# Performance work log

Measured on AMD Instinct MI355X. Metric: run time of the kernel, lower is better.

Reference implementation:

```python
import jax, jax.numpy as jnp
import numpy as np

# Default DigitCaps config: reduced_votes=False, iter=1, softmax=False, tanh_like=False,
# l_thetas=[1.0], lr_som=1.0, radical=False, no normalization, no winner-ratio bookkeeping.
H, Wd, INPUT_F, INPUT_D = 12, 12, 32, 8
C, D, M = 10, 8, 4          # num_out_caps, vector_depth, transf_mat_for_each_caps
LR, THETA = 1.0, 1.0


def setup_inputs() -> dict:
    key = jax.random.key(0)
    k1, k2, k3 = jax.random.split(key, 3)
    B = 128
    inputs = jax.random.normal(k1, (B, H, Wd, INPUT_F, INPUT_D), dtype=jnp.float32)
    J = H * Wd * INPUT_F  # 4608 positions
    # he_normal over fan_in = INPUT_D
    W = jax.random.normal(k2, (J, INPUT_D, D * M), dtype=jnp.float32) * jnp.sqrt(2.0 / INPUT_D)
    digit_caps = jax.random.uniform(k3, (C, D), minval=-1.0, maxval=1.0, dtype=jnp.float32)
    return {"inputs": inputs, "W": W, "digit_caps": digit_caps}


def reference(inputs, W, digit_caps):
    B = inputs.shape[0]
    J = H * Wd * INPUT_F
    x = inputs.reshape(B, J, INPUT_D)
    # per-position transform: [B,J,input_d] x [J,input_d,D*M] -> [B,J,D*M]
    u = jnp.einsum('bji,jik->bjk', x, W)
    N = J * M
    u = u.reshape(B, N, D)  # votes (broadcast over C instead of tiling)

    # similarities[b,n,c] = <u[b,n], digit_caps[c]>
    sims = jnp.einsum('bnd,cd->bnc', u, digit_caps)
    winners = jnp.argmax(sims, axis=-1)  # [B, N] int

    # sparse_updates = one_hot(winners) * (u - digit_caps) * lr * theta;
    # updates = mean over (B, N). Computed via segment-sum (honors winner sparsity).
    flat_w = winners.reshape(-1)
    flat_u = u.reshape(-1, D)
    seg_u = jax.ops.segment_sum(flat_u, flat_w, num_segments=C)          # [C, D]
    counts = jnp.zeros((C,), jnp.float32).at[flat_w].add(1.0)            # [C]
    denom = jnp.float32(B * N)
    updates = (seg_u - counts[:, None] * digit_caps) * (LR * THETA) / denom

    digit_caps_new = digit_caps + updates  # assign_add happens before final sims

    sims_final = jnp.einsum('bnd,cd->bnc', u, digit_caps_new)
    output = jnp.mean(sims_final, axis=-2)  # [B, C]
    return output, digit_caps_new
```

## Files before the change

### kernel.cpp

```cpp
#include <hip/hip_runtime.h>


#define J_POS 4608
#define SEGSTRIDE 97
#define NSEG 32
#define SSTRIDE 513
#define NSREP 8
#define NVOTES 18432.0f
#define DENOM  2359296.0f
#define SEG_SCALE 32768.0f
#define INV_SEG_SCALE 3.0517578125e-5f
#define OFF_PART_SEG 64
#define OFF_PART_S   110656
#define OFF_S_FINAL  700480
#define OFF_SEG_PART_LL 350752

__global__ __launch_bounds__(256) void votes_kernel(
    const float* __restrict__ x,
    const float* __restrict__ w,
    const float* __restrict__ dc,
    int* __restrict__ part_seg,
    int* __restrict__ part_s,
    int* __restrict__ done)
{
    __shared__ int seg_lds[NSEG * SEGSTRIDE];
    __shared__ int s_lds[NSREP * SSTRIDE];

    const int t  = threadIdx.x;
    const int jg = blockIdx.x >> 1;
    const int h  = blockIdx.x & 1;
    const int j0 = jg * 8;

    if (blockIdx.x == 0 && t == 0) *done = 0;

    for (int i = t; i < NSEG * SEGSTRIDE; i += 256) seg_lds[i] = 0;
    for (int i = t; i < NSREP * SSTRIDE; i += 256) s_lds[i] = 0;

    const int jj   = t >> 5;
    const int m    = (t >> 3) & 3;
    const int brow = t & 7;
    const int j = j0 + jj;

    float4 wra[8], wrb[8];
    {
        const float* wp = w + (size_t)j * 256 + m * 8;
        #pragma unroll
        for (int i = 0; i < 8; ++i) {
            wra[i] = *(const float4*)(wp + i * 32);
            wrb[i] = *(const float4*)(wp + i * 32 + 4);
        }
    }
    float4 dca[10], dcb[10];
    #pragma unroll
    for (int c = 0; c < 10; ++c) {
        dca[c] = *(const float4*)(dc + c * 8);
        dcb[c] = *(const float4*)(dc + c * 8 + 4);
    }

    int* const segp = &seg_lds[((t >> 1) & (NSEG - 1)) * SEGSTRIDE];
    int* const sp = &s_lds[((t >> 3) & (NSREP - 1)) * SSTRIDE];

    __syncthreads();

    const int bbase = h * 64 + brow;
    float4 nx0, nx1, mx0, mx1;
    {
        const float* xp = x + ((size_t)bbase * J_POS + j) * 8;
        nx0 = *(const float4*)xp; nx1 = *(const float4*)(xp + 4);
        const float* xq = x + ((size_t)(bbase + 8) * J_POS + j) * 8;
        mx0 = *(const float4*)xq; mx1 = *(const float4*)(xq + 4);
    }

    #pragma unroll 1
    for (int it = 0; it < 8; ++it) {
        const int bl = it * 8 + brow;
        const float4 x0 = nx0, x1 = nx1;
        nx0 = mx0; nx1 = mx1;
        if (it < 6) {
            const float* xp = x + ((size_t)(bbase + (it + 2) * 8) * J_POS + j) * 8;
            mx0 = *(const float4*)xp;
            mx1 = *(const float4*)(xp + 4);
        }
        const float xf[8] = {x0.x,x0.y,x0.z,x0.w,x1.x,x1.y,x1.z,x1.w};

        float u[8] = {0,0,0,0,0,0,0,0};
        #pragma unroll
        for (int i = 0; i < 8; ++i) {
            const float xi = xf[i];
            u[0] += xi * wra[i].x; u[1] += xi * wra[i].y;
            u[2] += xi * wra[i].z; u[3] += xi * wra[i].w;
            u[4] += xi * wrb[i].x; u[5] += xi * wrb[i].y;
            u[6] += xi * wrb[i].z; u[7] += xi * wrb[i].w;
        }

        float best = -3.402823466e38f;
        int bc = 0;
        #pragma unroll
        for (int c = 0; c < 10; ++c) {
            const float sim = u[0]*dca[c].x + u[1]*dca[c].y + u[2]*dca[c].z + u[3]*dca[c].w
                            + u[4]*dcb[c].x + u[5]*dcb[c].y + u[6]*dcb[c].z + u[7]*dcb[c].w;
            if (sim > best) { best = sim; bc = c; }
        }

        const int o = bc * 9;
        const int sb = bl * 8;
        #pragma unroll
        for (int d = 0; d < 8; ++d) {
            const int q = __float2int_rn(u[d] * SEG_SCALE);
            atomicAdd(&segp[o + d], q);
            atomicAdd(&sp[sb + d], q);
        }
        atomicAdd(&segp[o + 8], 1);
    }

    __syncthreads();

    if (t < 90) {
        int v = 0;
        #pragma unroll
        for (int r = 0; r < NSEG; ++r) v += seg_lds[r * SEGSTRIDE + t];
        part_seg[blockIdx.x * 96 + t] = v;
    }
    #pragma unroll
    for (int e = t; e < 512; e += 256) {
        int v = 0;
        #pragma unroll
        for (int r = 0; r < NSREP; ++r) v += s_lds[r * SSTRIDE + e];
        part_s[(size_t)blockIdx.x * 512 + e] = v;
    }
}

__global__ __launch_bounds__(256) void reduce_final_kernel(
    const int* __restrict__ part_seg,
    const int* __restrict__ part_s,
    float* __restrict__ s_final,
    long long* __restrict__ seg_part,
    int* __restrict__ done,
    const float* __restrict__ dc,
    float* __restrict__ out)
{
    __shared__ long long red[64][5];
    __shared__ long long segred[2][96];
    __shared__ float dcn[80];
    __shared__ float sf[1024];
    __shared__ int lastflag;

    const int t = threadIdx.x;
    const int bid = blockIdx.x;

    if (bid < 16) {
        const int g0 = bid * 64;
        const int h = g0 >> 9;
        const int gl = t & 63, chunk = t >> 6;
        const int col = (g0 + gl) & 511;
        long long acc = 0;
        #pragma unroll 8
        for (int i = chunk * 144; i < chunk * 144 + 144; ++i)
            acc += part_s[(size_t)(2 * i + h) * 512 + col];
        red[gl][chunk] = acc;
        __syncthreads();
        if (t < 64) {
            const long long v = red[t][0] + red[t][1] + red[t][2] + red[t][3];
            __hip_atomic_store(&s_final[g0 + t], (float)v * INV_SEG_SCALE,
                               __ATOMIC_RELAXED, __HIP_MEMORY_SCOPE_AGENT);
        }
    } else {
        const int p = bid - 16;
        if (t < 192) {
            const int o = t % 96, rc = t / 96;
            long long acc = 0;
            const int r0 = p * 288 + rc * 144;
            #pragma unroll 8
            for (int i = r0; i < r0 + 144; ++i)
                acc += part_seg[(size_t)i * 96 + o];
            segred[rc][o] = acc;
        }
        __syncthreads();
        if (t < 96)
            __hip_atomic_store(&seg_part[p * 96 + t], segred[0][t] + segred[1][t],
                               __ATOMIC_RELAXED, __HIP_MEMORY_SCOPE_AGENT);
    }

    __threadfence();
    __syncthreads();
    if (t == 0) lastflag = (atomicAdd(done, 1) == 19) ? 1 : 0;
    __syncthreads();
    if (!lastflag) return;
    __threadfence();

    #pragma unroll
    for (int r = 0; r < 4; ++r) {
        const int i = r * 256 + t;
        const float v = __hip_atomic_load(&s_final[i], __ATOMIC_RELAXED,
                                          __HIP_MEMORY_SCOPE_AGENT);
        sf[i] = v * (1.0f / NVOTES);
    }
    if (t < 80) {
        const int c = t >> 3, d = t & 7;
        long long sv = 0, cv = 0;
        #pragma unroll
        for (int p = 0; p < 4; ++p) {
            sv += __hip_atomic_load(&seg_part[p * 96 + c * 9 + d], __ATOMIC_RELAXED,
                                    __HIP_MEMORY_SCOPE_AGENT);
            cv += __hip_atomic_load(&seg_part[p * 96 + c * 9 + 8], __ATOMIC_RELAXED,
                                    __HIP_MEMORY_SCOPE_AGENT);
        }
        const float d0 = dc[t];
        const float nd = d0 + ((float)sv * INV_SEG_SCALE - (float)cv * d0) * (1.0f / DENOM);
        dcn[t] = nd;
        out[1280 + t] = nd;
    }
    __syncthreads();

    #pragma unroll
    for (int r = 0; r < 5; ++r) {
        const int idx = r * 256 + t;
        const int b = idx / 10, c = idx - b * 10;
        float acc = 0.f;
        #pragma unroll
        for (int d = 0; d < 8; ++d) acc += sf[b * 8 + d] * dcn[c * 8 + d];
        out[idx] = acc;
    }
}

extern "C" void kernel_launch(void* const* d_in, const int* in_sizes, int n_in,
                              void* d_out, int out_size, void* d_ws, size_t ws_size,
                              hipStream_t stream) {
    const float* x  = (const float*)d_in[0];
    const float* w  = (const float*)d_in[1];
    const float* dc = (const float*)d_in[2];
    float* out = (float*)d_out;
    int*       done      = (int*)d_ws;
    int*       part_seg  = (int*)d_ws + OFF_PART_SEG;
    int*       part_s    = (int*)d_ws + OFF_PART_S;
    float*     s_final   = (float*)d_ws + OFF_S_FINAL;
    long long* seg_part  = (long long*)d_ws + OFF_SEG_PART_LL;

    votes_kernel<<<1152, 256, 0, stream>>>(x, w, dc, part_seg, part_s, done);
    reduce_final_kernel<<<20, 256, 0, stream>>>(part_seg, part_s, s_final,
                                                seg_part, done, dc, out);
}
```

Baseline: 101.4 us.

## Remap votes threads so DPP pre-reduces per-batch sums across capsule slots

Each votes block now covers all 128 batches for 8 positions, so the grid halves to 576 blocks and each thread runs 16 iterations. Threads are remapped so the 4 transform matrices m sit in adjacent lanes. A DPP quad reduction sums the quantized votes across m, and only one lane in four issues the per-batch LDS atomics. This cuts LDS atomic traffic on the s buffer by a factor of four and halves the partial rows the reduce kernel reads. The cost is a doubled s_lds footprint, which may lower occupancy, fewer blocks in flight, and x loads that are less coalesced under the new lane mapping.

```diff
diff --git a/kernel.cpp b/kernel.cpp
--- a/kernel.cpp
+++ b/kernel.cpp
@@ -4,16 +4,16 @@
 #define J_POS 4608
 #define SEGSTRIDE 97
 #define NSEG 32
-#define SSTRIDE 513
+#define SSTRIDE 1025
 #define NSREP 8
 #define NVOTES 18432.0f
 #define DENOM  2359296.0f
 #define SEG_SCALE 32768.0f
 #define INV_SEG_SCALE 3.0517578125e-5f
 #define OFF_PART_SEG 64
-#define OFF_PART_S   110656
-#define OFF_S_FINAL  700480
-#define OFF_SEG_PART_LL 350752
+#define OFF_PART_S   55360
+#define OFF_S_FINAL  645184
+#define OFF_SEG_PART_LL 323104
 
 __global__ __launch_bounds__(256) void votes_kernel(
     const float* __restrict__ x,
@@ -27,18 +27,16 @@
     __shared__ int s_lds[NSREP * SSTRIDE];
 
     const int t  = threadIdx.x;
-    const int jg = blockIdx.x >> 1;
-    const int h  = blockIdx.x & 1;
-    const int j0 = jg * 8;
+    const int j0 = blockIdx.x * 8;
 
     if (blockIdx.x == 0 && t == 0) *done = 0;
 
     for (int i = t; i < NSEG * SEGSTRIDE; i += 256) seg_lds[i] = 0;
     for (int i = t; i < NSREP * SSTRIDE; i += 256) s_lds[i] = 0;
 
-    const int jj   = t >> 5;
-    const int m    = (t >> 3) & 3;
-    const int brow = t & 7;
+    const int m    = t & 3;
+    const int jj   = (t >> 2) & 7;
+    const int brow = t >> 5;
     const int j = j0 + jj;
 
     float4 wra[8], wrb[8];
@@ -58,26 +56,25 @@
     }
 
     int* const segp = &seg_lds[((t >> 1) & (NSEG - 1)) * SEGSTRIDE];
-    int* const sp = &s_lds[((t >> 3) & (NSREP - 1)) * SSTRIDE];
-
-    __syncthreads();
-
-    const int bbase = h * 64 + brow;
+    int* const sp   = &s_lds[jj * SSTRIDE];
+
+    __syncthreads();
+
     float4 nx0, nx1, mx0, mx1;
     {
-        const float* xp = x + ((size_t)bbase * J_POS + j) * 8;
+        const float* xp = x + ((size_t)brow * J_POS + j) * 8;
         nx0 = *(const float4*)xp; nx1 = *(const float4*)(xp + 4);
-        const float* xq = x + ((size_t)(bbase + 8) * J_POS + j) * 8;
+        const float* xq = x + ((size_t)(8 + brow) * J_POS + j) * 8;
         mx0 = *(const float4*)xq; mx1 = *(const float4*)(xq + 4);
     }
 
     #pragma unroll 1
-    for (int it = 0; it < 8; ++it) {
+    for (int it = 0; it < 16; ++it) {
         const int bl = it * 8 + brow;
         const float4 x0 = nx0, x1 = nx1;
         nx0 = mx0; nx1 = mx1;
-        if (it < 6) {
-            const float* xp = x + ((size_t)(bbase + (it + 2) * 8) * J_POS + j) * 8;
+        if (it < 14) {
+            const float* xp = x + ((size_t)((it + 2) * 8 + brow) * J_POS + j) * 8;
             mx0 = *(const float4*)xp;
             mx1 = *(const float4*)(xp + 4);
         }
@@ -102,15 +99,28 @@
             if (sim > best) { best = sim; bc = c; }
         }
 
+        int q[8];
+        #pragma unroll
+        for (int d = 0; d < 8; ++d) q[d] = __float2int_rn(u[d] * SEG_SCALE);
+
         const int o = bc * 9;
-        const int sb = bl * 8;
+        #pragma unroll
+        for (int d = 0; d < 8; ++d) atomicAdd(&segp[o + d], q[d]);
+        atomicAdd(&segp[o + 8], 1);
+
+        int sq[8];
         #pragma unroll
         for (int d = 0; d < 8; ++d) {
-            const int q = __float2int_rn(u[d] * SEG_SCALE);
-            atomicAdd(&segp[o + d], q);
-            atomicAdd(&sp[sb + d], q);
-        }
-        atomicAdd(&segp[o + 8], 1);
+            int v = q[d];
+            v += __builtin_amdgcn_update_dpp(0, v, 0xB1, 0xF, 0xF, true);
+            v += __builtin_amdgcn_update_dpp(0, v, 0x4E, 0xF, 0xF, true);
+            sq[d] = v;
+        }
+        if (m == 0) {
+            const int sb = bl * 8;
+            #pragma unroll
+            for (int d = 0; d < 8; ++d) atomicAdd(&sp[sb + d], sq[d]);
+        }
     }
 
     __syncthreads();
@@ -122,11 +132,11 @@
         part_seg[blockIdx.x * 96 + t] = v;
     }
     #pragma unroll
-    for (int e = t; e < 512; e += 256) {
+    for (int e = t; e < 1024; e += 256) {
         int v = 0;
         #pragma unroll
         for (int r = 0; r < NSREP; ++r) v += s_lds[r * SSTRIDE + e];
-        part_s[(size_t)blockIdx.x * 512 + e] = v;
+        part_s[(size_t)blockIdx.x * 1024 + e] = v;
     }
 }
 
@@ -150,13 +160,12 @@
 
     if (bid < 16) {
         const int g0 = bid * 64;
-        const int h = g0 >> 9;
         const int gl = t & 63, chunk = t >> 6;
-        const int col = (g0 + gl) & 511;
+        const int col = g0 + gl;
         long long acc = 0;
         #pragma unroll 8
         for (int i = chunk * 144; i < chunk * 144 + 144; ++i)
-            acc += part_s[(size_t)(2 * i + h) * 512 + col];
+            acc += part_s[(size_t)i * 1024 + col];
         red[gl][chunk] = acc;
         __syncthreads();
         if (t < 64) {
@@ -169,9 +178,9 @@
         if (t < 192) {
             const int o = t % 96, rc = t / 96;
             long long acc = 0;
-            const int r0 = p * 288 + rc * 144;
+            const int r0 = p * 144 + rc * 72;
             #pragma unroll 8
-            for (int i = r0; i < r0 + 144; ++i)
+            for (int i = r0; i < r0 + 72; ++i)
                 acc += part_seg[(size_t)i * 96 + o];
             segred[rc][o] = acc;
         }
@@ -236,7 +245,7 @@
     float*     s_final   = (float*)d_ws + OFF_S_FINAL;
     long long* seg_part  = (long long*)d_ws + OFF_SEG_PART_LL;
 
-    votes_kernel<<<1152, 256, 0, stream>>>(x, w, dc, part_seg, part_s, done);
+    votes_kernel<<<576, 256, 0, stream>>>(x, w, dc, part_seg, part_s, done);
     reduce_final_kernel<<<20, 256, 0, stream>>>(part_seg, part_s, s_final,
                                                 seg_part, done, dc, out);
 }
```

Result: slower. 108.7 us (+7.1%).
